# Optimization experiments

Hardware: AMD Instinct MI355X
Metric: run time of the kernel (lower is better)

## Reference

```python
import jax, jax.numpy as jnp
import numpy as np

B, T, C = 4, 2048, 1024
L = 256
H = 16
HS = C // H  # 64

def setup_inputs() -> dict:
    key = jax.random.key(0)
    ks = jax.random.split(key, 6)
    s = 0.02
    return {
        "x": jax.random.normal(ks[0], (B, T, C), dtype=jnp.float32),
        "Wq": jax.random.normal(ks[1], (C, C), dtype=jnp.float32) * s,
        "W_kv_down": jax.random.normal(ks[2], (C, L), dtype=jnp.float32) * s,
        "W_k_up": jax.random.normal(ks[3], (L, C), dtype=jnp.float32) * s,
        "W_v_up": jax.random.normal(ks[4], (L, C), dtype=jnp.float32) * s,
        "W_out": jax.random.normal(ks[5], (C, C), dtype=jnp.float32) * s,
    }

def reference(x, Wq, W_kv_down, W_k_up, W_v_up, W_out):
    # x: [B,T,C]
    q = (x @ Wq).reshape(B, T, H, HS).transpose(0, 2, 1, 3)        # [B,H,T,HS]
    latent_kv = x @ W_kv_down                                       # [B,T,L]
    k = (latent_kv @ W_k_up).reshape(B, T, H, HS).transpose(0, 2, 1, 3)
    v = (latent_kv @ W_v_up).reshape(B, T, H, HS).transpose(0, 2, 1, 3)
    att = jnp.einsum('bhtd,bhsd->bhts', q, k) / jnp.sqrt(jnp.float32(HS))
    causal = jnp.tril(jnp.ones((T, T), dtype=bool))
    att = jnp.where(causal[None, None], att, jnp.float32(-jnp.inf))
    att = jax.nn.softmax(att, axis=-1)
    y = jnp.einsum('bhts,bhsd->bhtd', att, v)                       # [B,H,T,HS]
    y = y.transpose(0, 2, 1, 3).reshape(B, T, C)
    return y @ W_out
```

## Files before the change

kernel.cpp:

```cpp
#include <hip/hip_runtime.h>
#include <cstddef>
#include <cstdint>

#define BB 4
#define TT 2048
#define CC 1024
#define LL 256
#define HH 16
#define DD 64
#define QLD (CC + LL)

typedef __attribute__((ext_vector_type(8))) short s16x8;
typedef __attribute__((ext_vector_type(4))) float f32x4;

static __device__ inline unsigned short f2bf(float f) {
    union { float f; unsigned u; } v; v.f = f;
    unsigned r = v.u + 0x7fffu + ((v.u >> 16) & 1u);
    return (unsigned short)(r >> 16);
}

static __device__ inline float fast_exp2(float x) {
#if __has_builtin(__builtin_amdgcn_exp2f)
    return __builtin_amdgcn_exp2f(x);
#else
    return exp2f(x);
#endif
}

static __device__ inline unsigned pack_bf16_trunc(float lo, float hi) {
    union { float f; unsigned u; } a, b;
    a.f = lo; b.f = hi;
    return __builtin_amdgcn_perm(b.u, a.u, 0x07060302u);
}

#define GLDS16(g, l)                                             \
    __builtin_amdgcn_global_load_lds(                            \
        (__attribute__((address_space(1))) void*)(g),            \
        (__attribute__((address_space(3))) void*)(l), 16, 0, 0)

extern "C" __global__ __launch_bounds__(256)
void fused_cvt(const float* __restrict__ x, unsigned short* __restrict__ xb,
               const float* __restrict__ Wq, const float* __restrict__ Wkv,
               const float* __restrict__ Wk, const float* __restrict__ Wv,
               const float* __restrict__ Wo,
               unsigned short* __restrict__ W1t, unsigned short* __restrict__ W2t,
               unsigned short* __restrict__ Wot, float qscale) {
    __shared__ unsigned short Ts[64][72];
    const int t = threadIdx.x;
    int blk = blockIdx.x;
    if (blk < 8192) {
        const int i = blk * 256 + t;
        const float4 v = ((const float4*)x)[i];
        ushort4 o;
        o.x = f2bf(v.x); o.y = f2bf(v.y); o.z = f2bf(v.z); o.w = f2bf(v.w);
        ((ushort4*)xb)[i] = o;
        return;
    }
    blk -= 8192;
    const float* W; unsigned short* Wt; int K, N; float scale; int tile;
    if (blk < 256)      { W = Wq;  Wt = W1t;                      K = CC; N = CC; scale = qscale; tile = blk; }
    else if (blk < 320) { W = Wkv; Wt = W1t + (size_t)CC * CC;    K = CC; N = LL; scale = 1.f;    tile = blk - 256; }
    else if (blk < 384) { W = Wk;  Wt = W2t;                      K = LL; N = CC; scale = 1.f;    tile = blk - 320; }
    else if (blk < 448) { W = Wv;  Wt = W2t + (size_t)CC * LL;    K = LL; N = CC; scale = 1.f;    tile = blk - 384; }
    else                { W = Wo;  Wt = Wot;                      K = CC; N = CC; scale = 1.f;    tile = blk - 448; }
    const int ktiles = K >> 6;
    const int k0 = (tile % ktiles) * 64, n0 = (tile / ktiles) * 64;
#pragma unroll
    for (int l = 0; l < 4; ++l) {
        const int idx = t + l * 256;
        const int r = idx >> 4, c4 = (idx & 15) * 4;
        const float4 v = *(const float4*)(W + (size_t)(k0 + r) * N + n0 + c4);
        Ts[c4 + 0][r] = f2bf(v.x * scale); Ts[c4 + 1][r] = f2bf(v.y * scale);
        Ts[c4 + 2][r] = f2bf(v.z * scale); Ts[c4 + 3][r] = f2bf(v.w * scale);
    }
    __syncthreads();
#pragma unroll
    for (int l = 0; l < 2; ++l) {
        const int idx = t + l * 256;
        const int n = idx >> 3, seg = idx & 7;
        *(s16x8*)(Wt + (size_t)(n0 + n) * K + k0 + seg * 8) = *(const s16x8*)&Ts[n][seg * 8];
    }
}

template <int MODE>
__global__ __launch_bounds__(256)
void bgemm(const unsigned short* __restrict__ A, const unsigned short* __restrict__ Bt,
           void* __restrict__ Cv, void* __restrict__ Cv2,
           int M, int N, int K, int lda, int ldc) {
    __shared__ unsigned short As[128][64];
    __shared__ unsigned short Bs[128][64];
    const int t = threadIdx.x;
    const int w = t >> 6, lane = t & 63, quad = lane >> 4, l16 = lane & 15;
    const int wm = w & 1, wn = w >> 1;
    const int row0 = blockIdx.y * 128, col0 = blockIdx.x * 128;
    const int sr = lane >> 3;
    const int sc = ((lane & 7) ^ sr) * 8;

    f32x4 acc[4][4];
#pragma unroll
    for (int i = 0; i < 4; ++i)
#pragma unroll
        for (int j = 0; j < 4; ++j) acc[i][j] = (f32x4){0.f, 0.f, 0.f, 0.f};

    const unsigned short* Ab = A + (size_t)(row0 + w * 32 + sr) * lda + sc;
    const unsigned short* Bb = Bt + (size_t)(col0 + w * 32 + sr) * K + sc;

    for (int k0 = 0; k0 < K; k0 += 64) {
#pragma unroll
        for (int c = 0; c < 4; ++c) {
            GLDS16(Ab + (size_t)(c * 8) * lda + k0, &As[w * 32 + c * 8][0]);
            GLDS16(Bb + (size_t)(c * 8) * K + k0, &Bs[w * 32 + c * 8][0]);
        }
        __syncthreads();
#pragma unroll
        for (int kk = 0; kk < 2; ++kk) {
            s16x8 af[4], bfr[4];
#pragma unroll
            for (int mt = 0; mt < 4; ++mt)
                af[mt] = *(const s16x8*)
                    &As[wm * 64 + mt * 16 + l16][((kk * 4 + quad) ^ (l16 & 7)) * 8];
#pragma unroll
            for (int nt = 0; nt < 4; ++nt)
                bfr[nt] = *(const s16x8*)
                    &Bs[wn * 64 + nt * 16 + l16][((kk * 4 + quad) ^ (l16 & 7)) * 8];
#pragma unroll
            for (int mt = 0; mt < 4; ++mt)
#pragma unroll
                for (int nt = 0; nt < 4; ++nt)
                    acc[mt][nt] = __builtin_amdgcn_mfma_f32_16x16x32_bf16(
                        af[mt], bfr[nt], acc[mt][nt], 0, 0, 0);
        }
        __syncthreads();
    }

    if constexpr (MODE == 0) {
        float* C = (float*)Cv;
#pragma unroll
        for (int mt = 0; mt < 4; ++mt)
#pragma unroll
            for (int nt = 0; nt < 4; ++nt)
#pragma unroll
                for (int r = 0; r < 4; ++r)
                    C[(size_t)(row0 + wm * 64 + mt * 16 + quad * 4 + r) * ldc +
                      col0 + wn * 64 + nt * 16 + l16] = acc[mt][nt][r];
    } else if constexpr (MODE == 1) {
        unsigned short* C = (unsigned short*)Cv;
#pragma unroll
        for (int mt = 0; mt < 4; ++mt)
#pragma unroll
            for (int nt = 0; nt < 4; ++nt)
#pragma unroll
                for (int r = 0; r < 4; ++r)
                    C[(size_t)(row0 + wm * 64 + mt * 16 + quad * 4 + r) * ldc +
                      col0 + wn * 64 + nt * 16 + l16] = f2bf(acc[mt][nt][r]);
    } else {
        if (col0 < CC) {
            unsigned short* C = (unsigned short*)Cv;
#pragma unroll
            for (int mt = 0; mt < 4; ++mt)
#pragma unroll
                for (int nt = 0; nt < 4; ++nt)
#pragma unroll
                    for (int r = 0; r < 4; ++r)
                        C[(size_t)(row0 + wm * 64 + mt * 16 + quad * 4 + r) * ldc +
                          col0 + wn * 64 + nt * 16 + l16] = f2bf(acc[mt][nt][r]);
        } else {
            __shared__ unsigned short Tb[64][136];
            unsigned short* vt = (unsigned short*)Cv2;
            const int b   = row0 >> 11;
            const int tl0 = row0 & 2047;
#pragma unroll
            for (int h = 0; h < 2; ++h) {
                if (wn == h) {
#pragma unroll
                    for (int mt = 0; mt < 4; ++mt)
#pragma unroll
                        for (int nt = 0; nt < 4; ++nt)
#pragma unroll
                            for (int r = 0; r < 4; ++r)
                                Tb[nt * 16 + l16][wm * 64 + mt * 16 + quad * 4 + r] =
                                    f2bf(acc[mt][nt][r]);
                }
                __syncthreads();
                const int head = ((col0 - CC) >> 6) + h;
#pragma unroll
                for (int l = 0; l < 4; ++l) {
                    const int idx = t + l * 256;
                    const int dv = idx >> 4, seg = idx & 15;
                    *(s16x8*)(vt + (((size_t)b * HH + head) * DD + dv) * TT + tl0 + seg * 8) =
                        *(const s16x8*)&Tb[dv][seg * 8];
                }
                __syncthreads();
            }
        }
    }
}

extern "C" __global__ __launch_bounds__(256, 4)
void mla_attn2(const unsigned short* __restrict__ q,
               const unsigned short* __restrict__ k,
               const unsigned short* __restrict__ vt,
               unsigned short* __restrict__ y) {
    __shared__ unsigned short Ks[2][64][64];
    __shared__ unsigned short Vs[2][64][64];

    const int bh = blockIdx.x;
    const int qt2 = (gridDim.y - 1) - blockIdx.y;
    const int b = bh >> 4, h = bh & 15;
    const int t0 = qt2 * 128;
    const int t = threadIdx.x;
    const int w = t >> 6, lane = t & 63, quad = lane >> 4, l16 = lane & 15;
    const int qw0 = t0 + w * 32;
    const int swz = ((lane & 7) ^ ((lane >> 3) & 7)) * 8;
    const int lrow = lane >> 3;

    const unsigned short* kb0 = k + ((size_t)b * TT) * CC + h * DD;
    const unsigned short* vb0 = vt + ((size_t)(b * HH + h)) * DD * TT;

    s16x8 qf[2][2];
#pragma unroll
    for (int qs = 0; qs < 2; ++qs)
#pragma unroll
        for (int kh = 0; kh < 2; ++kh)
            qf[qs][kh] = *(const s16x8*)(q + ((size_t)b * TT + qw0 + qs * 16 + l16) * QLD +
                                         h * DD + kh * 32 + quad * 8);

    f32x4 o[2][4];
    float lsum[2] = {0.f, 0.f};
#pragma unroll
    for (int qs = 0; qs < 2; ++qs)
#pragma unroll
        for (int nt = 0; nt < 4; ++nt) o[qs][nt] = (f32x4){0.f, 0.f, 0.f, 0.f};

    const int nkt = 2 * qt2 + 2;

#define STAGE_KV(kt_, bi_)                                                     \
    do {                                                                       \
        const int s0_ = (kt_) * 64;                                            \
        _Pragma("unroll")                                                      \
        for (int c = 0; c < 2; ++c) {                                          \
            const int g = w * 2 + c;                                           \
            const int row = g * 8 + lrow;                                      \
            GLDS16(kb0 + (size_t)(s0_ + row) * CC + swz, &Ks[bi_][g * 8][0]);  \
            GLDS16(vb0 + (size_t)row * TT + s0_ + swz, &Vs[bi_][g * 8][0]);    \
        }                                                                      \
    } while (0)

    STAGE_KV(0, 0);
    __syncthreads();

    for (int kt = 0; kt < nkt; ++kt) {
        const int cur = kt & 1;
        if (kt + 1 < nkt) STAGE_KV(kt + 1, cur ^ 1);

        const int s0 = kt * 64;
        if (s0 <= qw0 + 31) {
            const unsigned short (*Kc)[64] = Ks[cur];
            const unsigned short (*Vc)[64] = Vs[cur];
            f32x4 st[2][4];
#pragma unroll
            for (int nt = 0; nt < 4; ++nt) {
                const int key = nt * 16 + l16;
                const s16x8 kf0 = *(const s16x8*)&Kc[key][((0 + quad) ^ (l16 & 7)) * 8];
                const s16x8 kf1 = *(const s16x8*)&Kc[key][((4 + quad) ^ (l16 & 7)) * 8];
#pragma unroll
                for (int qs = 0; qs < 2; ++qs) {
                    f32x4 acc = (f32x4){0.f, 0.f, 0.f, 0.f};
                    acc = __builtin_amdgcn_mfma_f32_16x16x32_bf16(kf0, qf[qs][0], acc, 0, 0, 0);
                    acc = __builtin_amdgcn_mfma_f32_16x16x32_bf16(kf1, qf[qs][1], acc, 0, 0, 0);
                    st[qs][nt] = acc;
                }
            }

            const bool maskedTile = (s0 + 63 > qw0);
            s16x8 pf[2][2];
#pragma unroll
            for (int qs = 0; qs < 2; ++qs) {
                const int qidx = qw0 + qs * 16 + l16;
                unsigned pc[4][2];
                float tsum = 0.f;
#pragma unroll
                for (int nt = 0; nt < 4; ++nt) {
                    const int key0 = s0 + nt * 16 + quad * 4;
                    float p[4];
#pragma unroll
                    for (int r = 0; r < 4; ++r) {
                        float sv = st[qs][nt][r];
                        if (maskedTile && (key0 + r > qidx)) sv = -1e30f;
                        p[r] = fast_exp2(sv);
                    }
                    tsum += (p[0] + p[1]) + (p[2] + p[3]);
                    pc[nt][0] = pack_bf16_trunc(p[0], p[1]);
                    pc[nt][1] = pack_bf16_trunc(p[2], p[3]);
                }
                lsum[qs] += tsum;
#pragma unroll
                for (int kh = 0; kh < 2; ++kh) {
                    auto s0a = __builtin_amdgcn_permlane32_swap(
                        (int)pc[2 * kh + 0][0], (int)pc[2 * kh + 1][0], false, false);
                    auto w02 = __builtin_amdgcn_permlane16_swap(s0a[0], s0a[1], false, false);
                    auto s1a = __builtin_amdgcn_permlane32_swap(
                        (int)pc[2 * kh + 0][1], (int)pc[2 * kh + 1][1], false, false);
                    auto w13 = __builtin_amdgcn_permlane16_swap(s1a[0], s1a[1], false, false);
                    union { unsigned u[4]; s16x8 v; } fu;
                    fu.u[0] = (unsigned)w02[0];
                    fu.u[1] = (unsigned)w13[0];
                    fu.u[2] = (unsigned)w02[1];
                    fu.u[3] = (unsigned)w13[1];
                    pf[qs][kh] = fu.v;
                }
            }

#pragma unroll
            for (int nt = 0; nt < 4; ++nt) {
                const int dv = nt * 16 + l16;
                const s16x8 vf0 = *(const s16x8*)&Vc[dv][((0 + quad) ^ (l16 & 7)) * 8];
                const s16x8 vf1 = *(const s16x8*)&Vc[dv][((4 + quad) ^ (l16 & 7)) * 8];
#pragma unroll
                for (int qs = 0; qs < 2; ++qs) {
                    o[qs][nt] = __builtin_amdgcn_mfma_f32_16x16x32_bf16(pf[qs][0], vf0,
                                                                        o[qs][nt], 0, 0, 0);
                    o[qs][nt] = __builtin_amdgcn_mfma_f32_16x16x32_bf16(pf[qs][1], vf1,
                                                                        o[qs][nt], 0, 0, 0);
                }
            }
        }
        __syncthreads();
    }

    float lfull[2];
#pragma unroll
    for (int qs = 0; qs < 2; ++qs) {
        float s = lsum[qs];
        s += __shfl_xor(s, 16);
        s += __shfl_xor(s, 32);
        lfull[qs] = s;
    }

#pragma unroll
    for (int qs = 0; qs < 2; ++qs) {
#pragma unroll
        for (int r = 0; r < 4; ++r) {
            const float inv = 1.f / __shfl(lfull[qs], quad * 4 + r);
            unsigned short* yb = y + ((size_t)b * TT + qw0 + qs * 16 + quad * 4 + r) * CC +
                                 h * DD + l16;
#pragma unroll
            for (int nt = 0; nt < 4; ++nt)
                yb[nt * 16] = f2bf(o[qs][nt][r] * inv);
        }
    }
}

extern "C" void kernel_launch(void* const* d_in, const int* in_sizes, int n_in,
                              void* d_out, int out_size, void* d_ws, size_t ws_size,
                              hipStream_t stream) {
    const float* x   = (const float*)d_in[0];
    const float* Wq  = (const float*)d_in[1];
    const float* Wkv = (const float*)d_in[2];
    const float* Wk  = (const float*)d_in[3];
    const float* Wv  = (const float*)d_in[4];
    const float* Wo  = (const float*)d_in[5];
    float* out = (float*)d_out;

    const int M = BB * TT;
    unsigned short* p = (unsigned short*)d_ws;
    unsigned short* xb    = p; p += (size_t)M * CC;
    unsigned short* qlatb = p; p += (size_t)M * QLD;
    unsigned short* kb    = p; p += (size_t)M * CC;
    unsigned short* vtb   = p; p += (size_t)M * CC;
    unsigned short* yb    = p; p += (size_t)M * CC;
    unsigned short* W1t   = p; p += (size_t)QLD * CC;
    unsigned short* W2t   = p; p += (size_t)(2 * CC) * LL;
    unsigned short* Wot   = p; p += (size_t)CC * CC;

    const float qscale = 0.125f * 1.44269504f;

    fused_cvt<<<8896, 256, 0, stream>>>(x, xb, Wq, Wkv, Wk, Wv, Wo,
                                        W1t, W2t, Wot, qscale);
    bgemm<1><<<dim3(QLD / 128, M / 128), 256, 0, stream>>>(
        xb, W1t, qlatb, nullptr, M, QLD, CC, CC, QLD);
    bgemm<3><<<dim3(2 * CC / 128, M / 128), 256, 0, stream>>>(
        qlatb + CC, W2t, kb, vtb, M, 2 * CC, LL, QLD, CC);
    mla_attn2<<<dim3(BB * HH, TT / 128), 256, 0, stream>>>(qlatb, kb, vtb, yb);
    bgemm<0><<<dim3(CC / 128, M / 128), 256, 0, stream>>>(
        yb, Wot, out, nullptr, M, CC, CC, CC, CC);
}
```

Measured before the change: 234.2 us.

## Use single-buffered 128-key KV tiles with setprio instead of double-buffered 64-key tiles

Replaces the double-buffered 64-key K/V staging with one 128-key tile loaded per iteration, then processed as two 64-key halves. This halves the number of loop iterations and barriers and raises MFMA priority around the compute via s_setprio. In exchange, loads no longer overlap compute, since each load is followed by a barrier before use. The V layout becomes 64x128 with a new swizzle.

Result: slower. 248.7 us (+6.2%).

```diff
diff --git a/kernel.cpp b/kernel.cpp
--- a/kernel.cpp
+++ b/kernel.cpp
@@ -201,8 +201,8 @@
                const unsigned short* __restrict__ k,
                const unsigned short* __restrict__ vt,
                unsigned short* __restrict__ y) {
-    __shared__ unsigned short Ks[2][64][64];
-    __shared__ unsigned short Vs[2][64][64];
+    __shared__ unsigned short Ks[128][64];
+    __shared__ unsigned short Vs[64][128];
 
     const int bh = blockIdx.x;
     const int qt2 = (gridDim.y - 1) - blockIdx.y;
@@ -211,8 +211,8 @@
     const int t = threadIdx.x;
     const int w = t >> 6, lane = t & 63, quad = lane >> 4, l16 = lane & 15;
     const int qw0 = t0 + w * 32;
-    const int swz = ((lane & 7) ^ ((lane >> 3) & 7)) * 8;
-    const int lrow = lane >> 3;
+    const int lrow8 = lane >> 3;
+    const int swzk = ((lane & 7) ^ lrow8) * 8;
 
     const unsigned short* kb0 = k + ((size_t)b * TT) * CC + h * DD;
     const unsigned short* vb0 = vt + ((size_t)(b * HH + h)) * DD * TT;
@@ -232,99 +232,100 @@
 #pragma unroll
         for (int nt = 0; nt < 4; ++nt) o[qs][nt] = (f32x4){0.f, 0.f, 0.f, 0.f};
 
-    const int nkt = 2 * qt2 + 2;
-
-#define STAGE_KV(kt_, bi_)                                                     \
-    do {                                                                       \
-        const int s0_ = (kt_) * 64;                                            \
-        _Pragma("unroll")                                                      \
-        for (int c = 0; c < 2; ++c) {                                          \
-            const int g = w * 2 + c;                                           \
-            const int row = g * 8 + lrow;                                      \
-            GLDS16(kb0 + (size_t)(s0_ + row) * CC + swz, &Ks[bi_][g * 8][0]);  \
-            GLDS16(vb0 + (size_t)row * TT + s0_ + swz, &Vs[bi_][g * 8][0]);    \
-        }                                                                      \
-    } while (0)
-
-    STAGE_KV(0, 0);
-    __syncthreads();
-
+    const int nkt = qt2 + 1;
     for (int kt = 0; kt < nkt; ++kt) {
-        const int cur = kt & 1;
-        if (kt + 1 < nkt) STAGE_KV(kt + 1, cur ^ 1);
-
-        const int s0 = kt * 64;
-        if (s0 <= qw0 + 31) {
-            const unsigned short (*Kc)[64] = Ks[cur];
-            const unsigned short (*Vc)[64] = Vs[cur];
-            f32x4 st[2][4];
-#pragma unroll
-            for (int nt = 0; nt < 4; ++nt) {
-                const int key = nt * 16 + l16;
-                const s16x8 kf0 = *(const s16x8*)&Kc[key][((0 + quad) ^ (l16 & 7)) * 8];
-                const s16x8 kf1 = *(const s16x8*)&Kc[key][((4 + quad) ^ (l16 & 7)) * 8];
+        const int s0 = kt * 128;
+#pragma unroll
+        for (int c = 0; c < 4; ++c) {
+            const int g = w * 4 + c;
+            GLDS16(kb0 + (size_t)(s0 + g * 8 + lrow8) * CC + swzk, &Ks[g * 8][0]);
+        }
+#pragma unroll
+        for (int c = 0; c < 4; ++c) {
+            const int g = w * 4 + c;
+            const int row = g * 4 + (lane >> 4);
+            const int ss = ((lane & 15) ^ (row & 7)) * 8;
+            GLDS16(vb0 + (size_t)row * TT + s0 + ss, &Vs[g * 4][0]);
+        }
+        __syncthreads();
+
+        __builtin_amdgcn_s_setprio(1);
+#pragma unroll
+        for (int hf = 0; hf < 2; ++hf) {
+            const int h0 = s0 + hf * 64;
+            if (h0 <= qw0 + 31) {
+                f32x4 st[2][4];
+#pragma unroll
+                for (int nt = 0; nt < 4; ++nt) {
+                    const int key = hf * 64 + nt * 16 + l16;
+                    const s16x8 kf0 = *(const s16x8*)&Ks[key][((0 + quad) ^ (l16 & 7)) * 8];
+                    const s16x8 kf1 = *(const s16x8*)&Ks[key][((4 + quad) ^ (l16 & 7)) * 8];
+#pragma unroll
+                    for (int qs = 0; qs < 2; ++qs) {
+                        f32x4 acc = (f32x4){0.f, 0.f, 0.f, 0.f};
+                        acc = __builtin_amdgcn_mfma_f32_16x16x32_bf16(kf0, qf[qs][0], acc, 0, 0, 0);
+                        acc = __builtin_amdgcn_mfma_f32_16x16x32_bf16(kf1, qf[qs][1], acc, 0, 0, 0);
+                        st[qs][nt] = acc;
+                    }
+                }
+
+                const bool maskedHalf = (h0 + 63 > qw0);
+                s16x8 pf[2][2];
 #pragma unroll
                 for (int qs = 0; qs < 2; ++qs) {
-                    f32x4 acc = (f32x4){0.f, 0.f, 0.f, 0.f};
-                    acc = __builtin_amdgcn_mfma_f32_16x16x32_bf16(kf0, qf[qs][0], acc, 0, 0, 0);
-                    acc = __builtin_amdgcn_mfma_f32_16x16x32_bf16(kf1, qf[qs][1], acc, 0, 0, 0);
-                    st[qs][nt] = acc;
+                    const int qidx = qw0 + qs * 16 + l16;
+                    unsigned pc[4][2];
+                    float tsum = 0.f;
+#pragma unroll
+                    for (int nt = 0; nt < 4; ++nt) {
+                        const int key0 = h0 + nt * 16 + quad * 4;
+                        float p[4];
+#pragma unroll
+                        for (int r = 0; r < 4; ++r) {
+                            float sv = st[qs][nt][r];
+                            if (maskedHalf && (key0 + r > qidx)) sv = -1e30f;
+                            p[r] = fast_exp2(sv);
+                        }
+                        tsum += (p[0] + p[1]) + (p[2] + p[3]);
+                        pc[nt][0] = pack_bf16_trunc(p[0], p[1]);
+                        pc[nt][1] = pack_bf16_trunc(p[2], p[3]);
+                    }
+                    lsum[qs] += tsum;
+#pragma unroll
+                    for (int kh = 0; kh < 2; ++kh) {
+                        auto s0a = __builtin_amdgcn_permlane32_swap(
+                            (int)pc[2 * kh + 0][0], (int)pc[2 * kh + 1][0], false, false);
+                        auto w02 = __builtin_amdgcn_permlane16_swap(s0a[0], s0a[1], false, false);
+                        auto s1a = __builtin_amdgcn_permlane32_swap(
+                            (int)pc[2 * kh + 0][1], (int)pc[2 * kh + 1][1], false, false);
+                        auto w13 = __builtin_amdgcn_permlane16_swap(s1a[0], s1a[1], false, false);
+                        union { unsigned u[4]; s16x8 v; } fu;
+                        fu.u[0] = (unsigned)w02[0];
+                        fu.u[1] = (unsigned)w13[0];
+                        fu.u[2] = (unsigned)w02[1];
+                        fu.u[3] = (unsigned)w13[1];
+                        pf[qs][kh] = fu.v;
+                    }
+                }
+
+#pragma unroll
+                for (int nt = 0; nt < 4; ++nt) {
+                    const int dv = nt * 16 + l16;
+                    const s16x8 vf0 = *(const s16x8*)
+                        &Vs[dv][((hf << 3) | ((0 + quad) ^ (l16 & 7))) * 8];
+                    const s16x8 vf1 = *(const s16x8*)
+                        &Vs[dv][((hf << 3) | ((4 + quad) ^ (l16 & 7))) * 8];
+#pragma unroll
+                    for (int qs = 0; qs < 2; ++qs) {
+                        o[qs][nt] = __builtin_amdgcn_mfma_f32_16x16x32_bf16(pf[qs][0], vf0,
+                                                                            o[qs][nt], 0, 0, 0);
+                        o[qs][nt] = __builtin_amdgcn_mfma_f32_16x16x32_bf16(pf[qs][1], vf1,
+                                                                            o[qs][nt], 0, 0, 0);
+                    }
                 }
             }
-
-            const bool maskedTile = (s0 + 63 > qw0);
-            s16x8 pf[2][2];
-#pragma unroll
-            for (int qs = 0; qs < 2; ++qs) {
-                const int qidx = qw0 + qs * 16 + l16;
-                unsigned pc[4][2];
-                float tsum = 0.f;
-#pragma unroll
-                for (int nt = 0; nt < 4; ++nt) {
-                    const int key0 = s0 + nt * 16 + quad * 4;
-                    float p[4];
-#pragma unroll
-                    for (int r = 0; r < 4; ++r) {
-                        float sv = st[qs][nt][r];
-                        if (maskedTile && (key0 + r > qidx)) sv = -1e30f;
-                        p[r] = fast_exp2(sv);
-                    }
-                    tsum += (p[0] + p[1]) + (p[2] + p[3]);
-                    pc[nt][0] = pack_bf16_trunc(p[0], p[1]);
-                    pc[nt][1] = pack_bf16_trunc(p[2], p[3]);
-                }
-                lsum[qs] += tsum;
-#pragma unroll
-                for (int kh = 0; kh < 2; ++kh) {
-                    auto s0a = __builtin_amdgcn_permlane32_swap(
-                        (int)pc[2 * kh + 0][0], (int)pc[2 * kh + 1][0], false, false);
-                    auto w02 = __builtin_amdgcn_permlane16_swap(s0a[0], s0a[1], false, false);
-                    auto s1a = __builtin_amdgcn_permlane32_swap(
-                        (int)pc[2 * kh + 0][1], (int)pc[2 * kh + 1][1], false, false);
-                    auto w13 = __builtin_amdgcn_permlane16_swap(s1a[0], s1a[1], false, false);
-                    union { unsigned u[4]; s16x8 v; } fu;
-                    fu.u[0] = (unsigned)w02[0];
-                    fu.u[1] = (unsigned)w13[0];
-                    fu.u[2] = (unsigned)w02[1];
-                    fu.u[3] = (unsigned)w13[1];
-                    pf[qs][kh] = fu.v;
-                }
-            }
-
-#pragma unroll
-            for (int nt = 0; nt < 4; ++nt) {
-                const int dv = nt * 16 + l16;
-                const s16x8 vf0 = *(const s16x8*)&Vc[dv][((0 + quad) ^ (l16 & 7)) * 8];
-                const s16x8 vf1 = *(const s16x8*)&Vc[dv][((4 + quad) ^ (l16 & 7)) * 8];
-#pragma unroll
-                for (int qs = 0; qs < 2; ++qs) {
-                    o[qs][nt] = __builtin_amdgcn_mfma_f32_16x16x32_bf16(pf[qs][0], vf0,
-                                                                        o[qs][nt], 0, 0, 0);
-                    o[qs][nt] = __builtin_amdgcn_mfma_f32_16x16x32_bf16(pf[qs][1], vf1,
-                                                                        o[qs][nt], 0, 0, 0);
-                }
-            }
-        }
+        }
+        __builtin_amdgcn_s_setprio(0);
         __syncthreads();
     }
 
```

## Replace LDS-staged attention with single-wave blocks loading K/V directly into registers

Applied to the files above, without the earlier changes.

The attention kernel changes from 256-thread blocks that stage K/V tiles through double-buffered shared memory into 64-thread single-wave blocks. Each block handles 64 queries and loads K and V fragments straight from global memory into registers each iteration. This removes LDS traffic and block-wide barriers and skips masked work more tightly on the causal diagonal. In exchange, K/V reuse across waves now depends only on cache, register pressure rises with four query sub-tiles per wave, and global loads are no longer overlapped with compute by explicit prefetch.

New measurement: 245.2 us. 4.7% more time.

```diff
diff --git a/kernel.cpp b/kernel.cpp
--- a/kernel.cpp
+++ b/kernel.cpp
@@ -196,141 +196,111 @@
     }
 }
 
-extern "C" __global__ __launch_bounds__(256, 4)
-void mla_attn2(const unsigned short* __restrict__ q,
+extern "C" __global__ __launch_bounds__(64, 2)
+void mla_attn3(const unsigned short* __restrict__ q,
                const unsigned short* __restrict__ k,
                const unsigned short* __restrict__ vt,
                unsigned short* __restrict__ y) {
-    __shared__ unsigned short Ks[2][64][64];
-    __shared__ unsigned short Vs[2][64][64];
-
     const int bh = blockIdx.x;
-    const int qt2 = (gridDim.y - 1) - blockIdx.y;
+    const int qt = (gridDim.y - 1) - blockIdx.y;
     const int b = bh >> 4, h = bh & 15;
-    const int t0 = qt2 * 128;
-    const int t = threadIdx.x;
-    const int w = t >> 6, lane = t & 63, quad = lane >> 4, l16 = lane & 15;
-    const int qw0 = t0 + w * 32;
-    const int swz = ((lane & 7) ^ ((lane >> 3) & 7)) * 8;
-    const int lrow = lane >> 3;
-
-    const unsigned short* kb0 = k + ((size_t)b * TT) * CC + h * DD;
-    const unsigned short* vb0 = vt + ((size_t)(b * HH + h)) * DD * TT;
-
-    s16x8 qf[2][2];
-#pragma unroll
-    for (int qs = 0; qs < 2; ++qs)
+    const int qw0 = qt * 64;
+    const int lane = threadIdx.x & 63;
+    const int quad = lane >> 4, l16 = lane & 15;
+
+    const unsigned short* kb = k + ((size_t)b * TT) * CC + h * DD + quad * 8;
+    const unsigned short* vb = vt + ((size_t)(b * HH + h)) * DD * TT + quad * 8;
+
+    s16x8 qf[4][2];
+#pragma unroll
+    for (int qs = 0; qs < 4; ++qs)
 #pragma unroll
         for (int kh = 0; kh < 2; ++kh)
             qf[qs][kh] = *(const s16x8*)(q + ((size_t)b * TT + qw0 + qs * 16 + l16) * QLD +
                                          h * DD + kh * 32 + quad * 8);
 
-    f32x4 o[2][4];
-    float lsum[2] = {0.f, 0.f};
-#pragma unroll
-    for (int qs = 0; qs < 2; ++qs)
+    f32x4 o[4][4];
+    float lsum[4] = {0.f, 0.f, 0.f, 0.f};
+#pragma unroll
+    for (int qs = 0; qs < 4; ++qs)
 #pragma unroll
         for (int nt = 0; nt < 4; ++nt) o[qs][nt] = (f32x4){0.f, 0.f, 0.f, 0.f};
 
-    const int nkt = 2 * qt2 + 2;
-
-#define STAGE_KV(kt_, bi_)                                                     \
-    do {                                                                       \
-        const int s0_ = (kt_) * 64;                                            \
-        _Pragma("unroll")                                                      \
-        for (int c = 0; c < 2; ++c) {                                          \
-            const int g = w * 2 + c;                                           \
-            const int row = g * 8 + lrow;                                      \
-            GLDS16(kb0 + (size_t)(s0_ + row) * CC + swz, &Ks[bi_][g * 8][0]);  \
-            GLDS16(vb0 + (size_t)row * TT + s0_ + swz, &Vs[bi_][g * 8][0]);    \
-        }                                                                      \
-    } while (0)
-
-    STAGE_KV(0, 0);
-    __syncthreads();
-
-    for (int kt = 0; kt < nkt; ++kt) {
-        const int cur = kt & 1;
-        if (kt + 1 < nkt) STAGE_KV(kt + 1, cur ^ 1);
-
+    for (int kt = 0; kt <= qt; ++kt) {
         const int s0 = kt * 64;
-        if (s0 <= qw0 + 31) {
-            const unsigned short (*Kc)[64] = Ks[cur];
-            const unsigned short (*Vc)[64] = Vs[cur];
-            f32x4 st[2][4];
+        s16x8 kf[4][2];
+#pragma unroll
+        for (int nt = 0; nt < 4; ++nt) {
+            const unsigned short* kr = kb + (size_t)(s0 + nt * 16 + l16) * CC;
+            kf[nt][0] = *(const s16x8*)(kr);
+            kf[nt][1] = *(const s16x8*)(kr + 32);
+        }
+        s16x8 vf[4][2];
+#pragma unroll
+        for (int nt = 0; nt < 4; ++nt) {
+            const unsigned short* vr = vb + (size_t)(nt * 16 + l16) * TT + s0;
+            vf[nt][0] = *(const s16x8*)(vr);
+            vf[nt][1] = *(const s16x8*)(vr + 32);
+        }
+
+        const bool diag = (kt == qt);
+#pragma unroll
+        for (int qs = 0; qs < 4; ++qs) {
+            f32x4 st[4];
 #pragma unroll
             for (int nt = 0; nt < 4; ++nt) {
-                const int key = nt * 16 + l16;
-                const s16x8 kf0 = *(const s16x8*)&Kc[key][((0 + quad) ^ (l16 & 7)) * 8];
-                const s16x8 kf1 = *(const s16x8*)&Kc[key][((4 + quad) ^ (l16 & 7)) * 8];
-#pragma unroll
-                for (int qs = 0; qs < 2; ++qs) {
-                    f32x4 acc = (f32x4){0.f, 0.f, 0.f, 0.f};
-                    acc = __builtin_amdgcn_mfma_f32_16x16x32_bf16(kf0, qf[qs][0], acc, 0, 0, 0);
-                    acc = __builtin_amdgcn_mfma_f32_16x16x32_bf16(kf1, qf[qs][1], acc, 0, 0, 0);
-                    st[qs][nt] = acc;
+                f32x4 a = (f32x4){0.f, 0.f, 0.f, 0.f};
+                a = __builtin_amdgcn_mfma_f32_16x16x32_bf16(kf[nt][0], qf[qs][0], a, 0, 0, 0);
+                a = __builtin_amdgcn_mfma_f32_16x16x32_bf16(kf[nt][1], qf[qs][1], a, 0, 0, 0);
+                st[nt] = a;
+            }
+            const int qidx = qw0 + qs * 16 + l16;
+            unsigned pc[4][2];
+            float ts = 0.f;
+#pragma unroll
+            for (int nt = 0; nt < 4; ++nt) {
+                const int key0 = s0 + nt * 16 + quad * 4;
+                float p[4];
+#pragma unroll
+                for (int r = 0; r < 4; ++r) {
+                    float sv = st[nt][r];
+                    if (diag && (key0 + r > qidx)) sv = -1e30f;
+                    p[r] = fast_exp2(sv);
                 }
-            }
-
-            const bool maskedTile = (s0 + 63 > qw0);
-            s16x8 pf[2][2];
-#pragma unroll
-            for (int qs = 0; qs < 2; ++qs) {
-                const int qidx = qw0 + qs * 16 + l16;
-                unsigned pc[4][2];
-                float tsum = 0.f;
-#pragma unroll
-                for (int nt = 0; nt < 4; ++nt) {
-                    const int key0 = s0 + nt * 16 + quad * 4;
-                    float p[4];
-#pragma unroll
-                    for (int r = 0; r < 4; ++r) {
-                        float sv = st[qs][nt][r];
-                        if (maskedTile && (key0 + r > qidx)) sv = -1e30f;
-                        p[r] = fast_exp2(sv);
-                    }
-                    tsum += (p[0] + p[1]) + (p[2] + p[3]);
-                    pc[nt][0] = pack_bf16_trunc(p[0], p[1]);
-                    pc[nt][1] = pack_bf16_trunc(p[2], p[3]);
-                }
-                lsum[qs] += tsum;
-#pragma unroll
-                for (int kh = 0; kh < 2; ++kh) {
-                    auto s0a = __builtin_amdgcn_permlane32_swap(
-                        (int)pc[2 * kh + 0][0], (int)pc[2 * kh + 1][0], false, false);
-                    auto w02 = __builtin_amdgcn_permlane16_swap(s0a[0], s0a[1], false, false);
-                    auto s1a = __builtin_amdgcn_permlane32_swap(
-                        (int)pc[2 * kh + 0][1], (int)pc[2 * kh + 1][1], false, false);
-                    auto w13 = __builtin_amdgcn_permlane16_swap(s1a[0], s1a[1], false, false);
-                    union { unsigned u[4]; s16x8 v; } fu;
-                    fu.u[0] = (unsigned)w02[0];
-                    fu.u[1] = (unsigned)w13[0];
-                    fu.u[2] = (unsigned)w02[1];
-                    fu.u[3] = (unsigned)w13[1];
-                    pf[qs][kh] = fu.v;
-                }
-            }
-
+                ts += (p[0] + p[1]) + (p[2] + p[3]);
+                pc[nt][0] = pack_bf16_trunc(p[0], p[1]);
+                pc[nt][1] = pack_bf16_trunc(p[2], p[3]);
+            }
+            lsum[qs] += ts;
+            s16x8 pf[2];
+#pragma unroll
+            for (int kh = 0; kh < 2; ++kh) {
+                auto sa = __builtin_amdgcn_permlane32_swap(
+                    (int)pc[2 * kh + 0][0], (int)pc[2 * kh + 1][0], false, false);
+                auto w02 = __builtin_amdgcn_permlane16_swap(sa[0], sa[1], false, false);
+                auto sb = __builtin_amdgcn_permlane32_swap(
+                    (int)pc[2 * kh + 0][1], (int)pc[2 * kh + 1][1], false, false);
+                auto w13 = __builtin_amdgcn_permlane16_swap(sb[0], sb[1], false, false);
+                union { unsigned u[4]; s16x8 v; } fu;
+                fu.u[0] = (unsigned)w02[0];
+                fu.u[1] = (unsigned)w13[0];
+                fu.u[2] = (unsigned)w02[1];
+                fu.u[3] = (unsigned)w13[1];
+                pf[kh] = fu.v;
+            }
 #pragma unroll
             for (int nt = 0; nt < 4; ++nt) {
-                const int dv = nt * 16 + l16;
-                const s16x8 vf0 = *(const s16x8*)&Vc[dv][((0 + quad) ^ (l16 & 7)) * 8];
-                const s16x8 vf1 = *(const s16x8*)&Vc[dv][((4 + quad) ^ (l16 & 7)) * 8];
-#pragma unroll
-                for (int qs = 0; qs < 2; ++qs) {
-                    o[qs][nt] = __builtin_amdgcn_mfma_f32_16x16x32_bf16(pf[qs][0], vf0,
-                                                                        o[qs][nt], 0, 0, 0);
-                    o[qs][nt] = __builtin_amdgcn_mfma_f32_16x16x32_bf16(pf[qs][1], vf1,
-                                                                        o[qs][nt], 0, 0, 0);
-                }
-            }
-        }
-        __syncthreads();
-    }
-
-    float lfull[2];
-#pragma unroll
-    for (int qs = 0; qs < 2; ++qs) {
+                o[qs][nt] = __builtin_amdgcn_mfma_f32_16x16x32_bf16(pf[0], vf[nt][0],
+                                                                    o[qs][nt], 0, 0, 0);
+                o[qs][nt] = __builtin_amdgcn_mfma_f32_16x16x32_bf16(pf[1], vf[nt][1],
+                                                                    o[qs][nt], 0, 0, 0);
+            }
+        }
+    }
+
+    float lfull[4];
+#pragma unroll
+    for (int qs = 0; qs < 4; ++qs) {
         float s = lsum[qs];
         s += __shfl_xor(s, 16);
         s += __shfl_xor(s, 32);
@@ -338,7 +308,7 @@
     }
 
 #pragma unroll
-    for (int qs = 0; qs < 2; ++qs) {
+    for (int qs = 0; qs < 4; ++qs) {
 #pragma unroll
         for (int r = 0; r < 4; ++r) {
             const float inv = 1.f / __shfl(lfull[qs], quad * 4 + r);
@@ -381,7 +351,7 @@
         xb, W1t, qlatb, nullptr, M, QLD, CC, CC, QLD);
     bgemm<3><<<dim3(2 * CC / 128, M / 128), 256, 0, stream>>>(
         qlatb + CC, W2t, kb, vtb, M, 2 * CC, LL, QLD, CC);
-    mla_attn2<<<dim3(BB * HH, TT / 128), 256, 0, stream>>>(qlatb, kb, vtb, yb);
+    mla_attn3<<<dim3(BB * HH, TT / 64), 64, 0, stream>>>(qlatb, kb, vtb, yb);
     bgemm<0><<<dim3(CC / 128, M / 128), 256, 0, stream>>>(
         yb, Wot, out, nullptr, M, CC, CC, CC, CC);
 }
```
